# Kernel optimization log

Measured on AMD Instinct MI355X. Metric: run time of the kernel, lower is better.

Reference implementation:

```python
import jax, jax.numpy as jnp
import numpy as np

MB, E, N, IN_HALF, HID, OUT = 32, 4, 512, 64, 128, 128
EPS = 1e-5


def setup_inputs() -> dict:
    key = jax.random.key(0)
    ks = jax.random.split(key, 24)
    x = jax.random.normal(ks[0], (MB, N, IN_HALF), jnp.float32)
    u = jax.random.uniform(ks[1], (MB, E, N, N), jnp.float32)
    a = (u < 0.02).astype(jnp.float32)
    adj = jnp.maximum(a, jnp.swapaxes(a, -1, -2))  # symmetric 0/1, forward's sym branch holds
    def lin(k, i, o):
        return jax.random.normal(k, (i, o), jnp.float32) / np.float32(np.sqrt(i))
    d = {"x": x, "adj": adj}
    in_dims = [IN_HALF, HID, HID]
    for l in range(3):
        d[f"w_self{l}"] = lin(ks[2 + 6 * l], in_dims[l], HID)
        d[f"b_self{l}"] = jnp.zeros((HID,), jnp.float32)
        d[f"w_edge{l}"] = lin(ks[3 + 6 * l], in_dims[l], HID * E)
        d[f"b_edge{l}"] = jnp.zeros((HID * E,), jnp.float32)
        d[f"bn{l}_g"] = jnp.ones((N,), jnp.float32)
        d[f"bn{l}_b"] = jnp.zeros((N,), jnp.float32)
    d["w1"] = lin(ks[20], HID, HID)
    d["b1"] = jnp.zeros((HID,), jnp.float32)
    d["bn_f_g"] = jnp.ones((N,), jnp.float32)
    d["bn_f_b"] = jnp.zeros((N,), jnp.float32)
    d["w2"] = lin(ks[21], HID, OUT)
    d["b2"] = jnp.zeros((OUT,), jnp.float32)
    return d


def _rescale_adj(adj):
    # zero the diagonal, then normalize each column by total neighbor count
    n = adj.shape[-1]
    adj = adj * (1.0 - jnp.eye(n, dtype=adj.dtype))
    deg = adj.sum(axis=(1, 2))  # (mb, N): sum over edge types and rows
    inv = jnp.where(deg > 0, 1.0 / deg, 0.0)
    return inv[:, None, None, :] * adj


def _batchnorm_nodes(h, g, b):
    # torch BatchNorm1d(n_node) on (B, N, D): per-node stats over (B, D), biased var
    m = h.mean(axis=(0, 2), keepdims=True)
    v = ((h - m) ** 2).mean(axis=(0, 2), keepdims=True)
    return (h - m) / jnp.sqrt(v + EPS) * g[None, :, None] + b[None, :, None]


def _graph_conv(h, na, w_self, b_self, w_edge, b_edge):
    mb, n, _ = h.shape
    hs = h @ w_self + b_self  # (mb, N, out)
    m = (h @ w_edge + b_edge).reshape(mb, n, HID, E)  # (mb, N, out, E)
    # fused: per-edge-type adj matmul + sum over edge types, no (mb,E,N,out) blowup
    hr = jnp.einsum('benm,bmoe->bno', na, m)
    return hs + hr


def reference(x, adj,
              w_self0, b_self0, w_edge0, b_edge0, bn0_g, bn0_b,
              w_self1, b_self1, w_edge1, b_edge1, bn1_g, bn1_b,
              w_self2, b_self2, w_edge2, b_edge2, bn2_g, bn2_b,
              w1, b1, bn_f_g, bn_f_b, w2, b2):
    # adj is symmetric by construction -> forward's adj_sym == adj
    na = _rescale_adj(adj)  # identical across layers; computed once
    h = x
    layers = [
        (w_self0, b_self0, w_edge0, b_edge0, bn0_g, bn0_b),
        (w_self1, b_self1, w_edge1, b_edge1, bn1_g, bn1_b),
        (w_self2, b_self2, w_edge2, b_edge2, bn2_g, bn2_b),
    ]
    for ws, bs, we, be, g, b in layers:
        h = _graph_conv(h, na, ws, bs, we, be)
        h = _batchnorm_nodes(h, g, b)
        h = jax.nn.relu(h)
    h = h @ w1 + b1
    h = _batchnorm_nodes(h, bn_f_g, bn_f_b)
    h = jax.nn.relu(h)
    h = h @ w2 + b2
    return h
```

## Files before the change

### kernel.cpp

```cpp
#include <hip/hip_runtime.h>
#include <stdint.h>


typedef float  f32x4  __attribute__((ext_vector_type(4)));
typedef __bf16 bf16x8 __attribute__((ext_vector_type(8)));
typedef __bf16 bf16x4 __attribute__((ext_vector_type(4)));
typedef unsigned short ushort8v __attribute__((ext_vector_type(8)));
typedef uint32_t uint4v __attribute__((ext_vector_type(4)));

#define MBATCH 32
#define ETYPES 4
#define NNODE  512
#define HIDD   128

#define GLB(p) (const __attribute__((address_space(1))) uint32_t*)(p)
#define LDSp(p) (__attribute__((address_space(3))) uint32_t*)(p)

#define WP_S0 0
#define WP_E0 8192
#define WP_S1 40960
#define WP_E1 57344
#define WP_S2 122880
#define WP_E2 139264
#define WP_W1 204800
#define WP_W2 221184

struct Params {
  const float* x;
  const float* adj;
  const float* wself[3]; const float* bself[3];
  const float* wedge[3]; const float* bedge[3];
  const float* bng[3];   const float* bnb[3];
  const float* w1; const float* b1;
  const float* bnfg; const float* bnfb;
  const float* w2; const float* b2;
  __bf16* mmp; float* hs; __bf16* part;
  __bf16* hb0; __bf16* hb1;
  uint32_t* bm; float* degp; __bf16* wp;
  float* out;
};

__device__ void pack_phase(const float* __restrict__ adj, uint32_t* __restrict__ bm,
                           float* __restrict__ degp, int bid, int t, int nbl) {
  int wave = t >> 6, lane = t & 63;
  for (int rg = bid; rg < 16384; rg += nbl) {
    int r = rg * 4 + wave;
    int b = r >> 11, e = (r >> 9) & 3, n = r & 511;
    const float* row = adj + (long)r * 512;
    uint32_t myw = 0;
#pragma unroll
    for (int i = 0; i < 8; ++i) {
      uint64_t bal = __ballot(row[i * 64 + lane] != 0.f);
      uint32_t lo = (uint32_t)bal, hi = (uint32_t)(bal >> 32);
      if ((lane >> 1) == i) myw = (lane & 1) ? hi : lo;
    }
    if (lane == (n >> 5)) myw &= ~(1u << (n & 31));
    int pc = (lane < 16) ? __popc(myw) : 0;
    pc += __shfl_down(pc, 8);
    pc += __shfl_down(pc, 4);
    pc += __shfl_down(pc, 2);
    pc += __shfl_down(pc, 1);
    if (lane < 16) bm[(long)r * 16 + lane] = myw;
    if (lane == 0) degp[e * 16384 + b * 512 + n] = (float)pc;
  }
}

__device__ void prep_phase(const Params& P, int bid, int t, int nbl) {
  const float* Ws[8] = {P.wself[0], P.wedge[0], P.wself[1], P.wedge[1],
                        P.wself[2], P.wedge[2], P.w1, P.w2};
  const int Kt[8]  = {64, 64, 128, 128, 128, 128, 128, 128};
  const int NB[8]  = {2, 8, 2, 8, 2, 8, 2, 2};
  const int OFF[8] = {WP_S0, WP_E0, WP_S1, WP_E1, WP_S2, WP_E2, WP_W1, WP_W2};
#pragma unroll
  for (int wid = 0; wid < 8; ++wid) {
    int K = Kt[wid], nblk = NB[wid];
    int tot = K * nblk * 64;
    for (int gid = bid * 256 + t; gid < tot; gid += nbl * 256) {
      int c = gid & 63;
      int k = (gid >> 6) % K;
      int blk = (gid >> 6) / K;
      int edge = (nblk == 8);
      int WS = edge ? 512 : 128;
      int col = edge ? (((blk & 1) * 64 + c) * 4 + (blk >> 1)) : (blk * 64 + c);
      P.wp[OFF[wid] + (long)blk * K * 64 + (k >> 3) * 512 + c * 8 + (k & 7)] =
          (__bf16)Ws[wid][k * WS + col];
    }
  }
}

template <int K, bool F32IN>
__device__ void gemm_phase(char* smem, const void* __restrict__ hv,
                           const __bf16* __restrict__ wp_self,
                           const float* __restrict__ bias_self,
                           const __bf16* __restrict__ wp_edge,
                           const float* __restrict__ bias_edge,
                           const float* __restrict__ degp,
                           float* __restrict__ outF, __bf16* __restrict__ mmp,
                           int ntiles, int bid, int t, int nbl) {
  __bf16 (*Hl)[K + 8] = (__bf16(*)[K + 8])smem;
  __bf16* Wl = (__bf16*)(smem + 64 * (K + 8) * 2);
  int wave = t >> 6, lane = t & 63, l15 = lane & 15, q = lane >> 4;
  for (int tile = bid; tile < ntiles; tile += nbl) {
    __syncthreads();
    int g0 = (tile & 255) * 64;
    int by = tile >> 8;
    bool edge = by >= 2;
    {
      const __bf16* wblk = edge ? (wp_edge + (long)(by - 2) * K * 64)
                                : (wp_self + (long)by * K * 64);
      const char* g = (const char*)wblk;
#pragma unroll
      for (int i = 0; i < K / 32; ++i) {
        __builtin_amdgcn_global_load_lds(GLB(g + i * 4096 + wave * 1024 + lane * 16),
                                         LDSp((char*)Wl + i * 4096 + wave * 1024),
                                         16, 0, 0);
      }
    }
    for (int idx = t; idx < 64 * (K / 8); idx += 256) {
      int r = idx / (K / 8), ch = idx % (K / 8);
      if (F32IN) {
        const float* xf = (const float*)hv;
        f32x4 a = *(const f32x4*)(xf + (long)(g0 + r) * K + ch * 8);
        f32x4 bq = *(const f32x4*)(xf + (long)(g0 + r) * K + ch * 8 + 4);
        bf16x8 o;
#pragma unroll
        for (int j = 0; j < 4; ++j) { o[j] = (__bf16)a[j]; o[4 + j] = (__bf16)bq[j]; }
        *(bf16x8*)&Hl[r][ch * 8] = o;
      } else {
        const __bf16* hb = (const __bf16*)hv;
        *(bf16x8*)&Hl[r][ch * 8] = *(const bf16x8*)(hb + (long)(g0 + r) * K + ch * 8);
      }
    }
    __syncthreads();
    f32x4 acc[4] = {};
#pragma unroll
    for (int kk = 0; kk < K / 32; ++kk) {
      bf16x8 af = *(const bf16x8*)&Hl[wave * 16 + l15][kk * 32 + q * 8];
#pragma unroll
      for (int c = 0; c < 4; ++c) {
        bf16x8 bfr = *(const bf16x8*)&Wl[((kk * 4 + q) * 64 + c * 16 + l15) * 8];
        acc[c] = __builtin_amdgcn_mfma_f32_16x16x32_bf16(af, bfr, acc[c], 0, 0, 0);
      }
    }
    if (!edge) {
      int c0 = by * 64;
#pragma unroll
      for (int c = 0; c < 4; ++c) {
        float bc = bias_self[c0 + c * 16 + l15];
#pragma unroll
        for (int i = 0; i < 4; ++i) {
          int g = g0 + wave * 16 + q * 4 + i;
          outF[(long)g * HIDD + c0 + c * 16 + l15] = acc[c][i] + bc;
        }
      }
    } else {
      int blk = by - 2;
      int e = blk >> 1, o0 = (blk & 1) * 64;
      float iv[4];
#pragma unroll
      for (int i = 0; i < 4; ++i) {
        int gg = g0 + wave * 16 + q * 4 + i;
        float d = degp[gg] + degp[16384 + gg] + degp[32768 + gg] + degp[49152 + gg];
        iv[i] = d > 0.f ? 1.f / d : 0.f;
      }
      int b4e  = (g0 >> 9) * 4 + e;
      int octg = ((g0 & 511) >> 3) + wave * 2 + (q >> 1);
      int j0   = (q & 1) * 4;
#pragma unroll
      for (int c = 0; c < 4; ++c) {
        int o = o0 + c * 16 + l15;
        float bc = bias_edge[o * 4 + e];
        bf16x4 v4;
#pragma unroll
        for (int i = 0; i < 4; ++i) v4[i] = (__bf16)((acc[c][i] + bc) * iv[i]);
        *(bf16x4*)(mmp + ((long)(b4e * 64 + octg) * HIDD + o) * 8 + j0) = v4;
      }
    }
  }
}

__device__ void spmm_phase(char* smem, const uint32_t* __restrict__ bm,
                           const __bf16* __restrict__ mmp,
                           __bf16* __restrict__ part, int bid, int t, int nbl) {
  __bf16* Bl = (__bf16*)smem;
  int wave = t >> 6, lane = t & 63, l15 = lane & 15, q = lane >> 4;
  for (int tl = bid; tl < 1024; tl += nbl) {
    int tile = tl >> 7;
    int eb   = tl & 127;
    int e = eb >> 5, b = eb & 31;
    int nt = tile >> 1, oc = tile & 1;
    int n0 = nt * 128, o0 = oc * 64;

    const uint32_t* bmr = bm + ((long)((b * 4 + e) * 512 + n0 + wave * 32 + l15)) * 16;
    uint32_t rm0[16], rm1[16];
#pragma unroll
    for (int i = 0; i < 4; ++i) {
      uint4v v0 = *(const uint4v*)(bmr + i * 4);
      uint4v v1 = *(const uint4v*)(bmr + 256 + i * 4);
      rm0[i * 4 + 0] = v0.x; rm0[i * 4 + 1] = v0.y; rm0[i * 4 + 2] = v0.z; rm0[i * 4 + 3] = v0.w;
      rm1[i * 4 + 0] = v1.x; rm1[i * 4 + 1] = v1.y; rm1[i * 4 + 2] = v1.z; rm1[i * 4 + 3] = v1.w;
    }

    f32x4 acc0[4] = {}, acc1[4] = {};
#pragma unroll 1
    for (int mc = 0; mc < 8; ++mc) {
      __syncthreads();
#pragma unroll
      for (int i = 0; i < 2; ++i) {
        int oct = wave * 2 + i;
        const char* g = (const char*)mmp +
            ((long)(b * 4 + e) * 65536 + mc * 8192 + oct * 1024 + o0 * 8) * 2;
        __builtin_amdgcn_global_load_lds(GLB(g + lane * 16),
                                         LDSp((char*)Bl + oct * 1024),
                                         16, 0, 0);
      }
      __syncthreads();
#pragma unroll
      for (int kk = 0; kk < 2; ++kk) {
        uint32_t bits0 = (rm0[mc * 2 + kk] >> (q * 8)) & 0xffu;
        uint32_t bits1 = (rm1[mc * 2 + kk] >> (q * 8)) & 0xffu;
        ushort8v a0, a1;
#pragma unroll
        for (int j = 0; j < 8; ++j) {
          a0[j] = (bits0 >> j & 1u) ? (unsigned short)0x3F80 : (unsigned short)0;
          a1[j] = (bits1 >> j & 1u) ? (unsigned short)0x3F80 : (unsigned short)0;
        }
        union { ushort8v u; bf16x8 v; } c0, c1; c0.u = a0; c1.u = a1;
#pragma unroll
        for (int c = 0; c < 4; ++c) {
          bf16x8 bfr = *(const bf16x8*)&Bl[((kk * 4 + q) * 64 + c * 16 + l15) * 8];
          acc0[c] = __builtin_amdgcn_mfma_f32_16x16x32_bf16(c0.v, bfr, acc0[c], 0, 0, 0);
          acc1[c] = __builtin_amdgcn_mfma_f32_16x16x32_bf16(c1.v, bfr, acc1[c], 0, 0, 0);
        }
      }
    }
    __bf16* dst = part + (long)(e * 32 + b) * NNODE * HIDD;
#pragma unroll
    for (int c = 0; c < 4; ++c) {
#pragma unroll
      for (int i = 0; i < 4; ++i) {
        int n = n0 + wave * 32 + q * 4 + i;
        int o = o0 + c * 16 + l15;
        dst[(long)n * HIDD + o] = (__bf16)acc0[c][i];
        dst[(long)(n + 16) * HIDD + o] = (__bf16)acc1[c][i];
      }
    }
  }
}

template <bool HASP>
__device__ void bnstat_phase(char* smem, const float* __restrict__ hs,
                             const __bf16* __restrict__ part,
                             const float* __restrict__ gg,
                             const float* __restrict__ bb,
                             __bf16* __restrict__ hb, int bid, int t, int nbl) {
  float* sm = (float*)smem;
  float* rs = (float*)(smem + 16384);
  float* rq = (float*)(smem + 17408);
  float* bc = (float*)(smem + 18432);
  int o4 = t & 31, bq = t >> 5;
  for (int n = bid; n < 512; n += nbl) {
    __syncthreads();
    float s = 0.f, sq = 0.f;
#pragma unroll
    for (int i = 0; i < 4; ++i) {
      int b = bq + i * 8;
      long base = ((long)b * NNODE + n) * HIDD + o4 * 4;
      f32x4 v = *(const f32x4*)(hs + base);
      if (HASP) {
#pragma unroll
        for (int e = 0; e < 4; ++e) {
          bf16x4 pv = *(const bf16x4*)(part + ((long)(e * 32 + b) * NNODE + n) * HIDD + o4 * 4);
#pragma unroll
          for (int j = 0; j < 4; ++j) v[j] += (float)pv[j];
        }
      }
      *(f32x4*)&sm[b * 128 + o4 * 4] = v;
#pragma unroll
      for (int j = 0; j < 4; ++j) { s += v[j]; sq += v[j] * v[j]; }
    }
    rs[t] = s; rq[t] = sq;
    __syncthreads();
    for (int off = 128; off > 0; off >>= 1) {
      if (t < off) { rs[t] += rs[t + off]; rq[t] += rq[t + off]; }
      __syncthreads();
    }
    if (t == 0) {
      float mean = rs[0] * (1.f / 4096.f);
      float var = rq[0] * (1.f / 4096.f) - mean * mean;
      float rstd = rsqrtf(var + 1e-5f);
      float sc = gg[n] * rstd;
      bc[0] = sc;
      bc[1] = bb[n] - mean * sc;
    }
    __syncthreads();
    float sc = bc[0], sh = bc[1];
#pragma unroll
    for (int i = 0; i < 4; ++i) {
      int b = bq + i * 8;
      f32x4 v = *(const f32x4*)&sm[b * 128 + o4 * 4];
      bf16x4 o;
#pragma unroll
      for (int j = 0; j < 4; ++j) {
        float x = v[j] * sc + sh;
        o[j] = (__bf16)(x > 0.f ? x : 0.f);
      }
      *(bf16x4*)(hb + ((long)b * NNODE + n) * HIDD + o4 * 4) = o;
    }
  }
}

__global__ __launch_bounds__(256) void g_packprep(Params P) {
  pack_phase(P.adj, P.bm, P.degp, blockIdx.x, threadIdx.x, gridDim.x);
  prep_phase(P, blockIdx.x, threadIdx.x, gridDim.x);
}
template <int K, bool F32IN>
__global__ __launch_bounds__(256) void g_gemm(const void* hv, const __bf16* wps,
                                              const float* bs, const __bf16* wpe,
                                              const float* be, const float* degp,
                                              float* outF, __bf16* mmp, int ntiles) {
  __shared__ __align__(16) char smem[64 * (K + 8) * 2 + K * 64 * 2];
  gemm_phase<K, F32IN>(smem, hv, wps, bs, wpe, be, degp, outF, mmp, ntiles,
                       blockIdx.x, threadIdx.x, gridDim.x);
}
__global__ __launch_bounds__(256) void g_spmm(const uint32_t* bm, const __bf16* mmp,
                                              __bf16* part) {
  __shared__ __align__(16) char smem[8192];
  spmm_phase(smem, bm, mmp, part, blockIdx.x, threadIdx.x, gridDim.x);
}
template <bool HASP>
__global__ __launch_bounds__(256) void g_bnstat(const float* hs, const __bf16* part,
                                                const float* gg, const float* bb,
                                                __bf16* hb) {
  __shared__ __align__(16) char smem[18448];
  bnstat_phase<HASP>(smem, hs, part, gg, bb, hb, blockIdx.x, threadIdx.x, gridDim.x);
}

extern "C" void kernel_launch(void* const* d_in, const int* in_sizes, int n_in,
                              void* d_out, int out_size, void* d_ws, size_t ws_size,
                              hipStream_t stream) {
  (void)in_sizes; (void)n_in; (void)out_size; (void)ws_size;
  Params P;
  P.x   = (const float*)d_in[0];
  P.adj = (const float*)d_in[1];
  for (int l = 0; l < 3; ++l) {
    P.wself[l] = (const float*)d_in[2 + 6 * l];
    P.bself[l] = (const float*)d_in[3 + 6 * l];
    P.wedge[l] = (const float*)d_in[4 + 6 * l];
    P.bedge[l] = (const float*)d_in[5 + 6 * l];
    P.bng[l]   = (const float*)d_in[6 + 6 * l];
    P.bnb[l]   = (const float*)d_in[7 + 6 * l];
  }
  P.w1   = (const float*)d_in[20];
  P.b1   = (const float*)d_in[21];
  P.bnfg = (const float*)d_in[22];
  P.bnfb = (const float*)d_in[23];
  P.w2   = (const float*)d_in[24];
  P.b2   = (const float*)d_in[25];

  char* ws = (char*)d_ws;
  P.mmp  = (__bf16*)ws;
  P.hs   = (float*)(ws + 16777216);
  P.part = (__bf16*)(ws + 25165824);
  P.hb0  = (__bf16*)(ws + 41943040);
  P.hb1  = (__bf16*)(ws + 46137344);
  P.bm   = (uint32_t*)(ws + 50331648);
  P.degp = (float*)(ws + 54525952);
  P.wp   = (__bf16*)(ws + 54788096);
  P.out  = (float*)d_out;

  g_packprep<<<16384, 256, 0, stream>>>(P);

  g_gemm<64, true><<<2560, 256, 0, stream>>>(P.x, P.wp + WP_S0, P.bself[0],
                                             P.wp + WP_E0, P.bedge[0], P.degp,
                                             P.hs, P.mmp, 2560);
  g_spmm<<<1024, 256, 0, stream>>>(P.bm, P.mmp, P.part);
  g_bnstat<true><<<512, 256, 0, stream>>>(P.hs, P.part, P.bng[0], P.bnb[0], P.hb0);

  g_gemm<128, false><<<2560, 256, 0, stream>>>(P.hb0, P.wp + WP_S1, P.bself[1],
                                               P.wp + WP_E1, P.bedge[1], P.degp,
                                               P.hs, P.mmp, 2560);
  g_spmm<<<1024, 256, 0, stream>>>(P.bm, P.mmp, P.part);
  g_bnstat<true><<<512, 256, 0, stream>>>(P.hs, P.part, P.bng[1], P.bnb[1], P.hb1);

  g_gemm<128, false><<<2560, 256, 0, stream>>>(P.hb1, P.wp + WP_S2, P.bself[2],
                                               P.wp + WP_E2, P.bedge[2], P.degp,
                                               P.hs, P.mmp, 2560);
  g_spmm<<<1024, 256, 0, stream>>>(P.bm, P.mmp, P.part);
  g_bnstat<true><<<512, 256, 0, stream>>>(P.hs, P.part, P.bng[2], P.bnb[2], P.hb0);

  g_gemm<128, false><<<512, 256, 0, stream>>>(P.hb0, P.wp + WP_W1, P.b1,
                                              nullptr, nullptr, P.degp,
                                              P.hs, nullptr, 512);
  g_bnstat<false><<<512, 256, 0, stream>>>(P.hs, nullptr, P.bnfg, P.bnfb, P.hb1);
  g_gemm<128, false><<<512, 256, 0, stream>>>(P.hb1, P.wp + WP_W2, P.b2,
                                              nullptr, nullptr, P.degp,
                                              P.out, nullptr, 512);
}
```

Baseline: 365.3 us.

## Fuse batchnorm into spmm epilogue and next gemm prologue, drop bnstat kernels

Removes the separate bnstat kernels. The spmm now loops over all four edge types inside one block, starting from hs and accumulating in registers, so the per-edge partial buffer and its reduction go away. Each block emits bf16 output plus per-node sum and sum-of-squares through atomics. The next gemm applies normalize and relu while loading its input, and the spmm gains double-buffered LDS staging of the message tiles. This cuts launches and global traffic, at the cost of float atomic nondeterminism, a single-pass variance formula, and fewer spmm blocks (512).

```diff
diff --git a/kernel.cpp b/kernel.cpp
--- a/kernel.cpp
+++ b/kernel.cpp
@@ -34,9 +34,8 @@
   const float* w1; const float* b1;
   const float* bnfg; const float* bnfb;
   const float* w2; const float* b2;
-  __bf16* mmp; float* hs; __bf16* part;
-  __bf16* hb0; __bf16* hb1;
-  uint32_t* bm; float* degp; __bf16* wp;
+  __bf16* mmp; float* hs; __bf16* hf; __bf16* hb;
+  uint32_t* bm; float* degp; __bf16* wp; float* stats;
   float* out;
 };
 
@@ -88,14 +87,19 @@
   }
 }
 
-template <int K, bool F32IN>
+template <int K, int INM, int OUTM>
 __device__ void gemm_phase(char* smem, const void* __restrict__ hv,
+                           const float* __restrict__ stin,
+                           const float* __restrict__ bg,
+                           const float* __restrict__ bb,
                            const __bf16* __restrict__ wp_self,
                            const float* __restrict__ bias_self,
                            const __bf16* __restrict__ wp_edge,
                            const float* __restrict__ bias_edge,
                            const float* __restrict__ degp,
-                           float* __restrict__ outF, __bf16* __restrict__ mmp,
+                           float* __restrict__ outF, __bf16* __restrict__ outB,
+                           float* __restrict__ stout,
+                           __bf16* __restrict__ mmp,
                            int ntiles, int bid, int t, int nbl) {
   __bf16 (*Hl)[K + 8] = (__bf16(*)[K + 8])smem;
   __bf16* Wl = (__bf16*)(smem + 64 * (K + 8) * 2);
@@ -118,7 +122,7 @@
     }
     for (int idx = t; idx < 64 * (K / 8); idx += 256) {
       int r = idx / (K / 8), ch = idx % (K / 8);
-      if (F32IN) {
+      if (INM == 0) {
         const float* xf = (const float*)hv;
         f32x4 a = *(const f32x4*)(xf + (long)(g0 + r) * K + ch * 8);
         f32x4 bq = *(const f32x4*)(xf + (long)(g0 + r) * K + ch * 8 + 4);
@@ -127,8 +131,21 @@
         for (int j = 0; j < 4; ++j) { o[j] = (__bf16)a[j]; o[4 + j] = (__bf16)bq[j]; }
         *(bf16x8*)&Hl[r][ch * 8] = o;
       } else {
-        const __bf16* hb = (const __bf16*)hv;
-        *(bf16x8*)&Hl[r][ch * 8] = *(const bf16x8*)(hb + (long)(g0 + r) * K + ch * 8);
+        int g = g0 + r, n = g & 511;
+        float s = stin[n * 2], sq = stin[n * 2 + 1];
+        float mean = s * (1.f / 4096.f);
+        float var = sq * (1.f / 4096.f) - mean * mean;
+        float rstd = rsqrtf(var + 1e-5f);
+        float sc = bg[n] * rstd, sh = bb[n] - mean * sc;
+        const __bf16* hbp = (const __bf16*)hv;
+        bf16x8 hvv = *(const bf16x8*)(hbp + (long)g * K + ch * 8);
+        bf16x8 o;
+#pragma unroll
+        for (int j = 0; j < 8; ++j) {
+          float x = (float)hvv[j] * sc + sh;
+          o[j] = (__bf16)(x > 0.f ? x : 0.f);
+        }
+        *(bf16x8*)&Hl[r][ch * 8] = o;
       }
     }
     __syncthreads();
@@ -144,13 +161,43 @@
     }
     if (!edge) {
       int c0 = by * 64;
-#pragma unroll
-      for (int c = 0; c < 4; ++c) {
-        float bc = bias_self[c0 + c * 16 + l15];
+      if (OUTM == 0) {
+#pragma unroll
+        for (int c = 0; c < 4; ++c) {
+          float bc = bias_self[c0 + c * 16 + l15];
+#pragma unroll
+          for (int i = 0; i < 4; ++i) {
+            int g = g0 + wave * 16 + q * 4 + i;
+            outF[(long)g * HIDD + c0 + c * 16 + l15] = acc[c][i] + bc;
+          }
+        }
+      } else {
+        float rs[4] = {}, rq[4] = {};
+#pragma unroll
+        for (int c = 0; c < 4; ++c) {
+          float bc = bias_self[c0 + c * 16 + l15];
+#pragma unroll
+          for (int i = 0; i < 4; ++i) {
+            int g = g0 + wave * 16 + q * 4 + i;
+            float x = acc[c][i] + bc;
+            __bf16 xb = (__bf16)x;
+            outB[(long)g * HIDD + c0 + c * 16 + l15] = xb;
+            float rv = (float)xb;
+            rs[i] += rv; rq[i] += rv * rv;
+          }
+        }
 #pragma unroll
         for (int i = 0; i < 4; ++i) {
-          int g = g0 + wave * 16 + q * 4 + i;
-          outF[(long)g * HIDD + c0 + c * 16 + l15] = acc[c][i] + bc;
+          float s = rs[i], sq = rq[i];
+          s += __shfl_xor(s, 1); s += __shfl_xor(s, 2);
+          s += __shfl_xor(s, 4); s += __shfl_xor(s, 8);
+          sq += __shfl_xor(sq, 1); sq += __shfl_xor(sq, 2);
+          sq += __shfl_xor(sq, 4); sq += __shfl_xor(sq, 8);
+          if (l15 == 0) {
+            int n = (g0 + wave * 16 + q * 4 + i) & 511;
+            atomicAdd(&stout[n * 2], s);
+            atomicAdd(&stout[n * 2 + 1], sq);
+          }
         }
       }
     } else {
@@ -181,16 +228,37 @@
 
 __device__ void spmm_phase(char* smem, const uint32_t* __restrict__ bm,
                            const __bf16* __restrict__ mmp,
-                           __bf16* __restrict__ part, int bid, int t, int nbl) {
-  __bf16* Bl = (__bf16*)smem;
+                           const float* __restrict__ hs,
+                           __bf16* __restrict__ hf, float* __restrict__ stout,
+                           int bid, int t) {
+  char* Bl0 = smem;
+  char* Bl1 = smem + 4096;
   int wave = t >> 6, lane = t & 63, l15 = lane & 15, q = lane >> 4;
-  for (int tl = bid; tl < 1024; tl += nbl) {
-    int tile = tl >> 7;
-    int eb   = tl & 127;
-    int e = eb >> 5, b = eb & 31;
-    int nt = tile >> 1, oc = tile & 1;
-    int n0 = nt * 128, o0 = oc * 64;
-
+  int b = bid >> 4, nt = (bid >> 2) & 3, oc = bid & 3;
+  int n0 = nt * 128, o0 = oc * 32;
+
+  f32x4 acc0[2], acc1[2];
+#pragma unroll
+  for (int c = 0; c < 2; ++c) {
+#pragma unroll
+    for (int i = 0; i < 4; ++i) {
+      long r0 = (long)b * NNODE + n0 + wave * 32 + q * 4 + i;
+      acc0[c][i] = hs[r0 * HIDD + o0 + c * 16 + l15];
+      acc1[c][i] = hs[(r0 + 16) * HIDD + o0 + c * 16 + l15];
+    }
+  }
+
+  auto stage = [&](int e, int mc, char* dst) {
+    const char* g = (const char*)mmp +
+        ((long)(b * 4 + e) * 65536 + (mc * 8 + wave * 2 + (lane >> 5)) * 1024 +
+         o0 * 8) * 2 + (lane & 31) * 16;
+    __builtin_amdgcn_global_load_lds(GLB(g), LDSp(dst + wave * 1024), 16, 0, 0);
+  };
+
+  stage(0, 0, Bl0);
+
+#pragma unroll 1
+  for (int e = 0; e < 4; ++e) {
     const uint32_t* bmr = bm + ((long)((b * 4 + e) * 512 + n0 + wave * 32 + l15)) * 16;
     uint32_t rm0[16], rm1[16];
 #pragma unroll
@@ -200,21 +268,22 @@
       rm0[i * 4 + 0] = v0.x; rm0[i * 4 + 1] = v0.y; rm0[i * 4 + 2] = v0.z; rm0[i * 4 + 3] = v0.w;
       rm1[i * 4 + 0] = v1.x; rm1[i * 4 + 1] = v1.y; rm1[i * 4 + 2] = v1.z; rm1[i * 4 + 3] = v1.w;
     }
-
-    f32x4 acc0[4] = {}, acc1[4] = {};
-#pragma unroll 1
+#pragma unroll
     for (int mc = 0; mc < 8; ++mc) {
-      __syncthreads();
-#pragma unroll
-      for (int i = 0; i < 2; ++i) {
-        int oct = wave * 2 + i;
-        const char* g = (const char*)mmp +
-            ((long)(b * 4 + e) * 65536 + mc * 8192 + oct * 1024 + o0 * 8) * 2;
-        __builtin_amdgcn_global_load_lds(GLB(g + lane * 16),
-                                         LDSp((char*)Bl + oct * 1024),
-                                         16, 0, 0);
-      }
-      __syncthreads();
+      char* cur = (mc & 1) ? Bl1 : Bl0;
+      char* nxt = (mc & 1) ? Bl0 : Bl1;
+      if (mc < 7) {
+        stage(e, mc + 1, nxt);
+        asm volatile("s_waitcnt vmcnt(1)" ::: "memory");
+      } else if (e < 3) {
+        stage(e + 1, 0, nxt);
+        asm volatile("s_waitcnt vmcnt(1)" ::: "memory");
+      } else {
+        asm volatile("s_waitcnt vmcnt(0)" ::: "memory");
+      }
+      __builtin_amdgcn_s_barrier();
+      asm volatile("" ::: "memory");
+      const __bf16* Bl = (const __bf16*)cur;
 #pragma unroll
       for (int kk = 0; kk < 2; ++kk) {
         uint32_t bits0 = (rm0[mc * 2 + kk] >> (q * 8)) & 0xffu;
@@ -225,115 +294,74 @@
           a0[j] = (bits0 >> j & 1u) ? (unsigned short)0x3F80 : (unsigned short)0;
           a1[j] = (bits1 >> j & 1u) ? (unsigned short)0x3F80 : (unsigned short)0;
         }
-        union { ushort8v u; bf16x8 v; } c0, c1; c0.u = a0; c1.u = a1;
-#pragma unroll
-        for (int c = 0; c < 4; ++c) {
-          bf16x8 bfr = *(const bf16x8*)&Bl[((kk * 4 + q) * 64 + c * 16 + l15) * 8];
-          acc0[c] = __builtin_amdgcn_mfma_f32_16x16x32_bf16(c0.v, bfr, acc0[c], 0, 0, 0);
-          acc1[c] = __builtin_amdgcn_mfma_f32_16x16x32_bf16(c1.v, bfr, acc1[c], 0, 0, 0);
-        }
-      }
-    }
-    __bf16* dst = part + (long)(e * 32 + b) * NNODE * HIDD;
-#pragma unroll
-    for (int c = 0; c < 4; ++c) {
-#pragma unroll
-      for (int i = 0; i < 4; ++i) {
-        int n = n0 + wave * 32 + q * 4 + i;
-        int o = o0 + c * 16 + l15;
-        dst[(long)n * HIDD + o] = (__bf16)acc0[c][i];
-        dst[(long)(n + 16) * HIDD + o] = (__bf16)acc1[c][i];
-      }
-    }
-  }
-}
-
-template <bool HASP>
-__device__ void bnstat_phase(char* smem, const float* __restrict__ hs,
-                             const __bf16* __restrict__ part,
-                             const float* __restrict__ gg,
-                             const float* __restrict__ bb,
-                             __bf16* __restrict__ hb, int bid, int t, int nbl) {
-  float* sm = (float*)smem;
-  float* rs = (float*)(smem + 16384);
-  float* rq = (float*)(smem + 17408);
-  float* bc = (float*)(smem + 18432);
-  int o4 = t & 31, bq = t >> 5;
-  for (int n = bid; n < 512; n += nbl) {
-    __syncthreads();
-    float s = 0.f, sq = 0.f;
+        union { ushort8v u; bf16x8 v; } c0u, c1u; c0u.u = a0; c1u.u = a1;
+#pragma unroll
+        for (int c = 0; c < 2; ++c) {
+          bf16x8 bfr = *(const bf16x8*)&Bl[((kk * 4 + q) * 32 + c * 16 + l15) * 8];
+          acc0[c] = __builtin_amdgcn_mfma_f32_16x16x32_bf16(c0u.v, bfr, acc0[c], 0, 0, 0);
+          acc1[c] = __builtin_amdgcn_mfma_f32_16x16x32_bf16(c1u.v, bfr, acc1[c], 0, 0, 0);
+        }
+      }
+      asm volatile("" ::: "memory");
+      __builtin_amdgcn_s_barrier();
+      asm volatile("" ::: "memory");
+    }
+  }
+
+  long gb = (long)b * NNODE;
+#pragma unroll
+  for (int rg = 0; rg < 2; ++rg) {
 #pragma unroll
     for (int i = 0; i < 4; ++i) {
-      int b = bq + i * 8;
-      long base = ((long)b * NNODE + n) * HIDD + o4 * 4;
-      f32x4 v = *(const f32x4*)(hs + base);
-      if (HASP) {
-#pragma unroll
-        for (int e = 0; e < 4; ++e) {
-          bf16x4 pv = *(const bf16x4*)(part + ((long)(e * 32 + b) * NNODE + n) * HIDD + o4 * 4);
-#pragma unroll
-          for (int j = 0; j < 4; ++j) v[j] += (float)pv[j];
-        }
-      }
-      *(f32x4*)&sm[b * 128 + o4 * 4] = v;
-#pragma unroll
-      for (int j = 0; j < 4; ++j) { s += v[j]; sq += v[j] * v[j]; }
-    }
-    rs[t] = s; rq[t] = sq;
-    __syncthreads();
-    for (int off = 128; off > 0; off >>= 1) {
-      if (t < off) { rs[t] += rs[t + off]; rq[t] += rq[t + off]; }
-      __syncthreads();
-    }
-    if (t == 0) {
-      float mean = rs[0] * (1.f / 4096.f);
-      float var = rq[0] * (1.f / 4096.f) - mean * mean;
-      float rstd = rsqrtf(var + 1e-5f);
-      float sc = gg[n] * rstd;
-      bc[0] = sc;
-      bc[1] = bb[n] - mean * sc;
-    }
-    __syncthreads();
-    float sc = bc[0], sh = bc[1];
-#pragma unroll
-    for (int i = 0; i < 4; ++i) {
-      int b = bq + i * 8;
-      f32x4 v = *(const f32x4*)&sm[b * 128 + o4 * 4];
-      bf16x4 o;
-#pragma unroll
-      for (int j = 0; j < 4; ++j) {
-        float x = v[j] * sc + sh;
-        o[j] = (__bf16)(x > 0.f ? x : 0.f);
-      }
-      *(bf16x4*)(hb + ((long)b * NNODE + n) * HIDD + o4 * 4) = o;
+      int n = n0 + wave * 32 + rg * 16 + q * 4 + i;
+      float s = 0.f, sq = 0.f;
+#pragma unroll
+      for (int c = 0; c < 2; ++c) {
+        float x = rg ? acc1[c][i] : acc0[c][i];
+        __bf16 xb = (__bf16)x;
+        hf[(gb + n) * HIDD + o0 + c * 16 + l15] = xb;
+        float rv = (float)xb;
+        s += rv; sq += rv * rv;
+      }
+      s += __shfl_xor(s, 1); s += __shfl_xor(s, 2);
+      s += __shfl_xor(s, 4); s += __shfl_xor(s, 8);
+      sq += __shfl_xor(sq, 1); sq += __shfl_xor(sq, 2);
+      sq += __shfl_xor(sq, 4); sq += __shfl_xor(sq, 8);
+      if (l15 == 0) {
+        atomicAdd(&stout[n * 2], s);
+        atomicAdd(&stout[n * 2 + 1], sq);
+      }
     }
   }
 }
 
 __global__ __launch_bounds__(256) void g_packprep(Params P) {
+  if (blockIdx.x == 0) {
+    for (int i = threadIdx.x; i < 4096; i += 256) P.stats[i] = 0.f;
+  }
   pack_phase(P.adj, P.bm, P.degp, blockIdx.x, threadIdx.x, gridDim.x);
   prep_phase(P, blockIdx.x, threadIdx.x, gridDim.x);
 }
-template <int K, bool F32IN>
-__global__ __launch_bounds__(256) void g_gemm(const void* hv, const __bf16* wps,
-                                              const float* bs, const __bf16* wpe,
-                                              const float* be, const float* degp,
-                                              float* outF, __bf16* mmp, int ntiles) {
+
+template <int K, int INM, int OUTM>
+__global__ __launch_bounds__(256) void g_gemm(const void* hv, const float* stin,
+                                              const float* bg, const float* bb,
+                                              const __bf16* wps, const float* bs,
+                                              const __bf16* wpe, const float* be,
+                                              const float* degp, float* outF,
+                                              __bf16* outB, float* stout,
+                                              __bf16* mmp, int ntiles) {
   __shared__ __align__(16) char smem[64 * (K + 8) * 2 + K * 64 * 2];
-  gemm_phase<K, F32IN>(smem, hv, wps, bs, wpe, be, degp, outF, mmp, ntiles,
-                       blockIdx.x, threadIdx.x, gridDim.x);
-}
+  gemm_phase<K, INM, OUTM>(smem, hv, stin, bg, bb, wps, bs, wpe, be, degp,
+                           outF, outB, stout, mmp, ntiles,
+                           blockIdx.x, threadIdx.x, gridDim.x);
+}
+
 __global__ __launch_bounds__(256) void g_spmm(const uint32_t* bm, const __bf16* mmp,
-                                              __bf16* part) {
+                                              const float* hs, __bf16* hf,
+                                              float* stout) {
   __shared__ __align__(16) char smem[8192];
-  spmm_phase(smem, bm, mmp, part, blockIdx.x, threadIdx.x, gridDim.x);
-}
-template <bool HASP>
-__global__ __launch_bounds__(256) void g_bnstat(const float* hs, const __bf16* part,
-                                                const float* gg, const float* bb,
-                                                __bf16* hb) {
-  __shared__ __align__(16) char smem[18448];
-  bnstat_phase<HASP>(smem, hs, part, gg, bb, hb, blockIdx.x, threadIdx.x, gridDim.x);
+  spmm_phase(smem, bm, mmp, hs, hf, stout, blockIdx.x, threadIdx.x);
 }
 
 extern "C" void kernel_launch(void* const* d_in, const int* in_sizes, int n_in,
@@ -359,41 +387,37 @@
   P.b2   = (const float*)d_in[25];
 
   char* ws = (char*)d_ws;
-  P.mmp  = (__bf16*)ws;
-  P.hs   = (float*)(ws + 16777216);
-  P.part = (__bf16*)(ws + 25165824);
-  P.hb0  = (__bf16*)(ws + 41943040);
-  P.hb1  = (__bf16*)(ws + 46137344);
-  P.bm   = (uint32_t*)(ws + 50331648);
-  P.degp = (float*)(ws + 54525952);
-  P.wp   = (__bf16*)(ws + 54788096);
-  P.out  = (float*)d_out;
+  P.mmp   = (__bf16*)ws;
+  P.hs    = (float*)(ws + 16777216);
+  P.hf    = (__bf16*)(ws + 25165824);
+  P.hb    = (__bf16*)(ws + 29360128);
+  P.bm    = (uint32_t*)(ws + 33554432);
+  P.degp  = (float*)(ws + 37748736);
+  P.wp    = (__bf16*)(ws + 38010880);
+  P.stats = (float*)(ws + 38486016);
+  P.out   = (float*)d_out;
 
   g_packprep<<<16384, 256, 0, stream>>>(P);
 
-  g_gemm<64, true><<<2560, 256, 0, stream>>>(P.x, P.wp + WP_S0, P.bself[0],
-                                             P.wp + WP_E0, P.bedge[0], P.degp,
-                                             P.hs, P.mmp, 2560);
-  g_spmm<<<1024, 256, 0, stream>>>(P.bm, P.mmp, P.part);
-  g_bnstat<true><<<512, 256, 0, stream>>>(P.hs, P.part, P.bng[0], P.bnb[0], P.hb0);
-
-  g_gemm<128, false><<<2560, 256, 0, stream>>>(P.hb0, P.wp + WP_S1, P.bself[1],
-                                               P.wp + WP_E1, P.bedge[1], P.degp,
-                                               P.hs, P.mmp, 2560);
-  g_spmm<<<1024, 256, 0, stream>>>(P.bm, P.mmp, P.part);
-  g_bnstat<true><<<512, 256, 0, stream>>>(P.hs, P.part, P.bng[1], P.bnb[1], P.hb1);
-
-  g_gemm<128, false><<<2560, 256, 0, stream>>>(P.hb1, P.wp + WP_S2, P.bself[2],
-                                               P.wp + WP_E2, P.bedge[2], P.degp,
-                                               P.hs, P.mmp, 2560);
-  g_spmm<<<1024, 256, 0, stream>>>(P.bm, P.mmp, P.part);
-  g_bnstat<true><<<512, 256, 0, stream>>>(P.hs, P.part, P.bng[2], P.bnb[2], P.hb0);
-
-  g_gemm<128, false><<<512, 256, 0, stream>>>(P.hb0, P.wp + WP_W1, P.b1,
-                                              nullptr, nullptr, P.degp,
-                                              P.hs, nullptr, 512);
-  g_bnstat<false><<<512, 256, 0, stream>>>(P.hs, nullptr, P.bnfg, P.bnfb, P.hb1);
-  g_gemm<128, false><<<512, 256, 0, stream>>>(P.hb1, P.wp + WP_W2, P.b2,
-                                              nullptr, nullptr, P.degp,
-                                              P.out, nullptr, 512);
-}
+  g_gemm<64, 0, 0><<<2560, 256, 0, stream>>>(P.x, nullptr, nullptr, nullptr,
+      P.wp + WP_S0, P.bself[0], P.wp + WP_E0, P.bedge[0], P.degp,
+      P.hs, nullptr, nullptr, P.mmp, 2560);
+  g_spmm<<<512, 256, 0, stream>>>(P.bm, P.mmp, P.hs, P.hf, P.stats);
+
+  g_gemm<128, 1, 0><<<2560, 256, 0, stream>>>(P.hf, P.stats, P.bng[0], P.bnb[0],
+      P.wp + WP_S1, P.bself[1], P.wp + WP_E1, P.bedge[1], P.degp,
+      P.hs, nullptr, nullptr, P.mmp, 2560);
+  g_spmm<<<512, 256, 0, stream>>>(P.bm, P.mmp, P.hs, P.hf, P.stats + 1024);
+
+  g_gemm<128, 1, 0><<<2560, 256, 0, stream>>>(P.hf, P.stats + 1024, P.bng[1], P.bnb[1],
+      P.wp + WP_S2, P.bself[2], P.wp + WP_E2, P.bedge[2], P.degp,
+      P.hs, nullptr, nullptr, P.mmp, 2560);
+  g_spmm<<<512, 256, 0, stream>>>(P.bm, P.mmp, P.hs, P.hf, P.stats + 2048);
+
+  g_gemm<128, 1, 1><<<512, 256, 0, stream>>>(P.hf, P.stats + 2048, P.bng[2], P.bnb[2],
+      P.wp + WP_W1, P.b1, nullptr, nullptr, P.degp,
+      nullptr, P.hb, P.stats + 3072, nullptr, 512);
+  g_gemm<128, 1, 0><<<512, 256, 0, stream>>>(P.hb, P.stats + 3072, P.bnfg, P.bnfb,
+      P.wp + WP_W2, P.b2, nullptr, nullptr, P.degp,
+      P.out, nullptr, nullptr, nullptr, 512);
+}
```

Result: slower. 444.6 us (+21.7%).

## Multi-buffer SpMM B tiles in LDS with asynchronous prefetch pipeline

Applied to the files above, without the earlier changes.

Replaces the single LDS buffer in the SpMM phase with a 4-slot ring and keeps three stages of global-to-LDS loads in flight. Explicit vmcnt waits plus one barrier per step replace the two __syncthreads per chunk, so loads overlap the MFMA work. The grid-stride loop is dropped and each block now handles exactly one tile, which assumes the launch uses 1024 blocks. LDS use per block grows from 8 KB to 32 KB, which may limit occupancy.

```diff
diff --git a/kernel.cpp b/kernel.cpp
--- a/kernel.cpp
+++ b/kernel.cpp
@@ -181,69 +181,78 @@
 
 __device__ void spmm_phase(char* smem, const uint32_t* __restrict__ bm,
                            const __bf16* __restrict__ mmp,
-                           __bf16* __restrict__ part, int bid, int t, int nbl) {
-  __bf16* Bl = (__bf16*)smem;
+                           __bf16* __restrict__ part, int bid, int t) {
   int wave = t >> 6, lane = t & 63, l15 = lane & 15, q = lane >> 4;
-  for (int tl = bid; tl < 1024; tl += nbl) {
-    int tile = tl >> 7;
-    int eb   = tl & 127;
-    int e = eb >> 5, b = eb & 31;
-    int nt = tile >> 1, oc = tile & 1;
-    int n0 = nt * 128, o0 = oc * 64;
-
-    const uint32_t* bmr = bm + ((long)((b * 4 + e) * 512 + n0 + wave * 32 + l15)) * 16;
-    uint32_t rm0[16], rm1[16];
+  int tile = bid >> 7;
+  int eb   = bid & 127;
+  int e = eb >> 5, b = eb & 31;
+  int nt = tile >> 1, oc = tile & 1;
+  int n0 = nt * 128, o0 = oc * 64;
+
+  const uint32_t* bmr = bm + ((long)((b * 4 + e) * 512 + n0 + wave * 32 + l15)) * 16;
+  uint32_t rm0[16], rm1[16];
+#pragma unroll
+  for (int i = 0; i < 4; ++i) {
+    uint4v v0 = *(const uint4v*)(bmr + i * 4);
+    uint4v v1 = *(const uint4v*)(bmr + 256 + i * 4);
+    rm0[i * 4 + 0] = v0.x; rm0[i * 4 + 1] = v0.y; rm0[i * 4 + 2] = v0.z; rm0[i * 4 + 3] = v0.w;
+    rm1[i * 4 + 0] = v1.x; rm1[i * 4 + 1] = v1.y; rm1[i * 4 + 2] = v1.z; rm1[i * 4 + 3] = v1.w;
+  }
+
+  auto stage = [&](int mc, char* dst) {
+#pragma unroll
+    for (int i = 0; i < 2; ++i) {
+      int oct = wave * 2 + i;
+      const char* g = (const char*)mmp +
+          ((long)(b * 4 + e) * 65536 + mc * 8192 + oct * 1024 + o0 * 8) * 2;
+      __builtin_amdgcn_global_load_lds(GLB(g + lane * 16),
+                                       LDSp(dst + oct * 1024), 16, 0, 0);
+    }
+  };
+
+  stage(0, smem);
+  stage(1, smem + 8192);
+  stage(2, smem + 16384);
+
+  f32x4 acc0[4] = {}, acc1[4] = {};
+#pragma unroll
+  for (int mc = 0; mc < 8; ++mc) {
+    if (mc <= 5)      asm volatile("s_waitcnt vmcnt(4)" ::: "memory");
+    else if (mc == 6) asm volatile("s_waitcnt vmcnt(2)" ::: "memory");
+    else              asm volatile("s_waitcnt vmcnt(0)" ::: "memory");
+    __builtin_amdgcn_s_barrier();
+    asm volatile("" ::: "memory");
+    if (mc < 5) stage(mc + 3, smem + ((mc + 3) & 3) * 8192);
+    const __bf16* Bl = (const __bf16*)(smem + (mc & 3) * 8192);
+#pragma unroll
+    for (int kk = 0; kk < 2; ++kk) {
+      uint32_t bits0 = (rm0[mc * 2 + kk] >> (q * 8)) & 0xffu;
+      uint32_t bits1 = (rm1[mc * 2 + kk] >> (q * 8)) & 0xffu;
+      ushort8v a0, a1;
+#pragma unroll
+      for (int j = 0; j < 8; ++j) {
+        a0[j] = (bits0 >> j & 1u) ? (unsigned short)0x3F80 : (unsigned short)0;
+        a1[j] = (bits1 >> j & 1u) ? (unsigned short)0x3F80 : (unsigned short)0;
+      }
+      union { ushort8v u; bf16x8 v; } c0, c1; c0.u = a0; c1.u = a1;
+#pragma unroll
+      for (int c = 0; c < 4; ++c) {
+        bf16x8 bfr = *(const bf16x8*)&Bl[((kk * 4 + q) * 64 + c * 16 + l15) * 8];
+        acc0[c] = __builtin_amdgcn_mfma_f32_16x16x32_bf16(c0.v, bfr, acc0[c], 0, 0, 0);
+        acc1[c] = __builtin_amdgcn_mfma_f32_16x16x32_bf16(c1.v, bfr, acc1[c], 0, 0, 0);
+      }
+    }
+  }
+
+  __bf16* dst = part + (long)(e * 32 + b) * NNODE * HIDD;
+#pragma unroll
+  for (int c = 0; c < 4; ++c) {
 #pragma unroll
     for (int i = 0; i < 4; ++i) {
-      uint4v v0 = *(const uint4v*)(bmr + i * 4);
-      uint4v v1 = *(const uint4v*)(bmr + 256 + i * 4);
-      rm0[i * 4 + 0] = v0.x; rm0[i * 4 + 1] = v0.y; rm0[i * 4 + 2] = v0.z; rm0[i * 4 + 3] = v0.w;
-      rm1[i * 4 + 0] = v1.x; rm1[i * 4 + 1] = v1.y; rm1[i * 4 + 2] = v1.z; rm1[i * 4 + 3] = v1.w;
-    }
-
-    f32x4 acc0[4] = {}, acc1[4] = {};
-#pragma unroll 1
-    for (int mc = 0; mc < 8; ++mc) {
-      __syncthreads();
-#pragma unroll
-      for (int i = 0; i < 2; ++i) {
-        int oct = wave * 2 + i;
-        const char* g = (const char*)mmp +
-            ((long)(b * 4 + e) * 65536 + mc * 8192 + oct * 1024 + o0 * 8) * 2;
-        __builtin_amdgcn_global_load_lds(GLB(g + lane * 16),
-                                         LDSp((char*)Bl + oct * 1024),
-                                         16, 0, 0);
-      }
-      __syncthreads();
-#pragma unroll
-      for (int kk = 0; kk < 2; ++kk) {
-        uint32_t bits0 = (rm0[mc * 2 + kk] >> (q * 8)) & 0xffu;
-        uint32_t bits1 = (rm1[mc * 2 + kk] >> (q * 8)) & 0xffu;
-        ushort8v a0, a1;
-#pragma unroll
-        for (int j = 0; j < 8; ++j) {
-          a0[j] = (bits0 >> j & 1u) ? (unsigned short)0x3F80 : (unsigned short)0;
-          a1[j] = (bits1 >> j & 1u) ? (unsigned short)0x3F80 : (unsigned short)0;
-        }
-        union { ushort8v u; bf16x8 v; } c0, c1; c0.u = a0; c1.u = a1;
-#pragma unroll
-        for (int c = 0; c < 4; ++c) {
-          bf16x8 bfr = *(const bf16x8*)&Bl[((kk * 4 + q) * 64 + c * 16 + l15) * 8];
-          acc0[c] = __builtin_amdgcn_mfma_f32_16x16x32_bf16(c0.v, bfr, acc0[c], 0, 0, 0);
-          acc1[c] = __builtin_amdgcn_mfma_f32_16x16x32_bf16(c1.v, bfr, acc1[c], 0, 0, 0);
-        }
-      }
-    }
-    __bf16* dst = part + (long)(e * 32 + b) * NNODE * HIDD;
-#pragma unroll
-    for (int c = 0; c < 4; ++c) {
-#pragma unroll
-      for (int i = 0; i < 4; ++i) {
-        int n = n0 + wave * 32 + q * 4 + i;
-        int o = o0 + c * 16 + l15;
-        dst[(long)n * HIDD + o] = (__bf16)acc0[c][i];
-        dst[(long)(n + 16) * HIDD + o] = (__bf16)acc1[c][i];
-      }
+      int n = n0 + wave * 32 + q * 4 + i;
+      int o = o0 + c * 16 + l15;
+      dst[(long)n * HIDD + o] = (__bf16)acc0[c][i];
+      dst[(long)(n + 16) * HIDD + o] = (__bf16)acc1[c][i];
     }
   }
 }
@@ -325,8 +334,8 @@
 }
 __global__ __launch_bounds__(256) void g_spmm(const uint32_t* bm, const __bf16* mmp,
                                               __bf16* part) {
-  __shared__ __align__(16) char smem[8192];
-  spmm_phase(smem, bm, mmp, part, blockIdx.x, threadIdx.x, gridDim.x);
+  __shared__ __align__(16) char smem[32768];
+  spmm_phase(smem, bm, mmp, part, blockIdx.x, threadIdx.x);
 }
 template <bool HASP>
 __global__ __launch_bounds__(256) void g_bnstat(const float* hs, const __bf16* part,
```

Result: faster. 351.7 us (-3.7%).
